# Kernel tuning notes

Hardware: AMD Instinct MI355X
Metric: run time of the kernel (lower is better)

Reference implementation:

```python
import jax, jax.numpy as jnp
import numpy as np

TRIM_RATIO = 0.1
B, N, D_IN, D_H, N_OUT, D_OUT = 64, 1024, 512, 1024, 10, 1


def setup_inputs() -> dict:
    key = jax.random.key(0)
    ks = jax.random.split(key, 10)
    X = jax.random.normal(ks[0], (B, N, D_IN), dtype=jnp.float32)
    # ragged valid lengths in [N//2, N]; guarantees num_valid > 2*k for trim_ratio=0.1
    lengths = jax.random.randint(ks[1], (B,), N // 2, N + 1)
    mask = (jnp.arange(N)[None, :] < lengths[:, None]).astype(jnp.float32)
    s_in, s_h = 1.0 / np.sqrt(D_IN), 1.0 / np.sqrt(D_H)
    W1 = jax.random.uniform(ks[2], (D_IN, D_H), jnp.float32, -s_in, s_in)
    b1 = jax.random.uniform(ks[3], (D_H,), jnp.float32, -s_in, s_in)
    W2 = jax.random.uniform(ks[4], (D_H, D_H), jnp.float32, -s_h, s_h)
    b2 = jax.random.uniform(ks[5], (D_H,), jnp.float32, -s_h, s_h)
    W3 = jax.random.uniform(ks[6], (D_H, D_H), jnp.float32, -s_h, s_h)
    b3 = jax.random.uniform(ks[7], (D_H,), jnp.float32, -s_h, s_h)
    W4 = jax.random.uniform(ks[8], (D_H, N_OUT * D_OUT), jnp.float32, -s_h, s_h)
    b4 = jax.random.uniform(ks[9], (N_OUT * D_OUT,), jnp.float32, -s_h, s_h)
    return {"X": X, "mask": mask, "W1": W1, "b1": b1, "W2": W2, "b2": b2,
            "W3": W3, "b3": b3, "W4": W4, "b4": b4}


def reference(X, mask, W1, b1, W2, b2, W3, b3, W4, b4):
    # encode MLP: [B,N,D_IN] -> [B,N,D_H]
    encoded = jax.nn.relu(jnp.einsum('bni,ih->bnh', X, W1) + b1) @ W2 + b2
    masked = encoded * mask[..., None]
    num_valid = mask.sum(axis=-1).astype(jnp.int32)                 # [B]
    k = (num_valid.astype(jnp.float32) * TRIM_RATIO).astype(jnp.int32)  # floor, as int()
    # push invalid rows to +inf so valid elements occupy the first num_valid slots after sort
    padded = jnp.where(mask[..., None] > 0, masked, jnp.inf)
    sorted_v = jnp.sort(padded, axis=1)                             # per-column sort, [B,N,D_H]
    pos = jnp.arange(N)[None, :]
    keep = (pos >= k[:, None]) & (pos < (num_valid - k)[:, None])   # [B,N]
    summed = jnp.sum(jnp.where(keep[..., None], sorted_v, 0.0), axis=1)  # [B,D_H]
    denom = (num_valid - 2 * k).astype(jnp.float32)[:, None]
    aggregated = summed / denom                                     # trimmed mean
    # decode MLP
    out = jax.nn.relu(aggregated @ W3 + b3) @ W4 + b4               # [B, N_OUT*D_OUT]
    out = out.reshape(-1, N_OUT, D_OUT).squeeze(-1)                 # [B, N_OUT]
    return out
```

## Files before the change

kernel.cpp:

```cpp
#include <hip/hip_runtime.h>


typedef _Float16 half8  __attribute__((ext_vector_type(8)));
typedef _Float16 half4v __attribute__((ext_vector_type(4)));
typedef float    floatx4 __attribute__((ext_vector_type(4)));

#define GLD_LDS(g, l)                                                                     \
  __builtin_amdgcn_global_load_lds((const __attribute__((address_space(1))) void*)(g),    \
                                   (__attribute__((address_space(3))) void*)(l), 16, 0, 0)

__global__ void prep_nv(const float* __restrict__ mask, int* __restrict__ nv_arr,
                        int* __restrict__ k_arr) {
  int b = blockIdx.x, lane = threadIdx.x;
  const float4* mp = (const float4*)(mask + (b << 10));
  float s = 0.f;
#pragma unroll
  for (int i = 0; i < 4; ++i) {
    float4 v = mp[lane + i * 64];
    s += v.x + v.y + v.z + v.w;
  }
#pragma unroll
  for (int off = 32; off > 0; off >>= 1) s += __shfl_xor(s, off, 64);
  if (lane == 0) {
    int nv = (int)(s + 0.5f);
    int kk = (int)((float)nv * 0.1f);
    nv_arr[b] = nv;
    k_arr[b] = kk;
  }
}

__device__ __forceinline__ void transpose_body(const float* __restrict__ W,
                                               _Float16* __restrict__ WT, int R, int C,
                                               int r0, int c0, _Float16 (*tile)[65]) {
  for (int i = threadIdx.x; i < 4096; i += 256) {
    int r = i >> 6, c = i & 63;
    tile[r][c] = (_Float16)W[(size_t)(r0 + r) * C + c0 + c];
  }
  __syncthreads();
  for (int i = threadIdx.x; i < 4096; i += 256) {
    int c = i >> 6, r = i & 63;
    WT[(size_t)(c0 + c) * R + r0 + r] = tile[r][c];
  }
}

__global__ __launch_bounds__(256) void preprocess(
    const float* __restrict__ X, _Float16* __restrict__ X16,
    const float* __restrict__ W1, _Float16* __restrict__ W1T,
    const float* __restrict__ W2, _Float16* __restrict__ W2T,
    const int* __restrict__ nv_arr) {
  __shared__ _Float16 tile[64][65];
  int bid = blockIdx.x;
  if (bid < 16384) {
    int n0 = (bid << 2) & 1023;
    int batch = bid >> 8;
    int nv = nv_arr[batch];
    if (n0 >= ((nv + 127) & ~127)) return;
    int i = (bid * 256 + threadIdx.x) * 8;
    float4 a = *(const float4*)(X + i);
    float4 c = *(const float4*)(X + i + 4);
    half8 h;
    h[0] = (_Float16)a.x; h[1] = (_Float16)a.y; h[2] = (_Float16)a.z; h[3] = (_Float16)a.w;
    h[4] = (_Float16)c.x; h[5] = (_Float16)c.y; h[6] = (_Float16)c.z; h[7] = (_Float16)c.w;
    *(half8*)(X16 + i) = h;
  } else if (bid < 16384 + 128) {
    int id = bid - 16384;
    transpose_body(W1, W1T, 512, 1024, (id & 7) * 64, (id >> 3) * 64, tile);
  } else {
    int id = bid - 16512;
    transpose_body(W2, W2T, 1024, 1024, (id & 15) * 64, (id >> 4) * 64, tile);
  }
}

template <int KDIM, int MODE>
__global__ __launch_bounds__(256, 3) void gemm_kernel_sm(
    const _Float16* __restrict__ Aop, const _Float16* __restrict__ Bop,
    const float* __restrict__ bias, const int* __restrict__ nv_arr,
    _Float16* __restrict__ outp) {
  __shared__ __align__(16) _Float16 ldsA[128 * 64];
  __shared__ __align__(16) _Float16 ldsB[128 * 64];
  int i0, j0;
  int bid = blockIdx.x;
  int fat = (((bid >> 6) << 3) | (bid & 7)) * 128;
  int thin = ((bid >> 3) & 7) * 128;
  if (MODE == 1) {
    i0 = thin; j0 = fat;
    if ((j0 & 1023) >= nv_arr[j0 >> 10]) return;
  } else {
    i0 = fat; j0 = thin;
    if ((i0 & 1023) >= nv_arr[i0 >> 10]) return;
  }
  const int t = threadIdx.x, lane = t & 63;
  const int wv = t >> 6, wi = wv & 1, wj = wv >> 1;
  const int lr = lane & 15, q = lane >> 4;

  floatx4 acc[4][4] = {};

  const int gch = (t & 7) ^ ((t >> 3) & 7);
  const _Float16* gA[4];
  const _Float16* gB[4];
  _Float16* lA[4];
  _Float16* lB[4];
#pragma unroll
  for (int r = 0; r < 4; ++r) {
    int row = r * 32 + (t >> 3);
    gA[r] = Aop + (size_t)(i0 + row) * KDIM + gch * 8;
    gB[r] = Bop + (size_t)(j0 + row) * KDIM + gch * 8;
    lA[r] = ldsA + (r * 256 + (t & ~63)) * 8;
    lB[r] = ldsB + (r * 256 + (t & ~63)) * 8;
  }

  int aoff[4], boff[4];
#pragma unroll
  for (int mi = 0; mi < 4; ++mi) {
    int row = wi * 64 + mi * 16 + lr;
    aoff[mi] = row * 64 + ((q ^ (row & 7)) * 8);
  }
#pragma unroll
  for (int nj = 0; nj < 4; ++nj) {
    int row = wj * 64 + nj * 16 + lr;
    boff[nj] = row * 64 + ((q ^ (row & 7)) * 8);
  }

  for (int kt = 0; kt < KDIM / 64; ++kt) {
#pragma unroll
    for (int r = 0; r < 4; ++r) GLD_LDS(gA[r], lA[r]);
#pragma unroll
    for (int r = 0; r < 4; ++r) GLD_LDS(gB[r], lB[r]);
#pragma unroll
    for (int r = 0; r < 4; ++r) { gA[r] += 64; gB[r] += 64; }
    __syncthreads();
#pragma unroll
    for (int kk = 0; kk < 2; ++kk) {
      half8 af[4], bf[4];
#pragma unroll
      for (int mi = 0; mi < 4; ++mi) af[mi] = *(const half8*)&ldsA[aoff[mi] ^ (kk * 32)];
#pragma unroll
      for (int nj = 0; nj < 4; ++nj) bf[nj] = *(const half8*)&ldsB[boff[nj] ^ (kk * 32)];
#pragma unroll
      for (int mi = 0; mi < 4; ++mi)
#pragma unroll
        for (int nj = 0; nj < 4; ++nj)
          acc[mi][nj] =
              __builtin_amdgcn_mfma_f32_16x16x32_f16(af[mi], bf[nj], acc[mi][nj], 0, 0, 0);
    }
    __syncthreads();
  }

  if (MODE == 1) {
#pragma unroll
    for (int mi = 0; mi < 4; ++mi) {
      int ih = i0 + wi * 64 + mi * 16 + q * 4;
      floatx4 bb = *(const floatx4*)&bias[ih];
#pragma unroll
      for (int nj = 0; nj < 4; ++nj) {
        int j = j0 + wj * 64 + nj * 16 + lr;
        floatx4 v = acc[mi][nj];
        half4v hv;
#pragma unroll
        for (int r = 0; r < 4; ++r) hv[r] = (_Float16)fmaxf(v[r] + bb[r], 0.f);
        *(half4v*)&outp[(size_t)j * 1024 + ih] = hv;
      }
    }
  } else {
#pragma unroll
    for (int nj = 0; nj < 4; ++nj) {
      int j = j0 + wj * 64 + nj * 16 + lr;
      float bj = bias[j];
#pragma unroll
      for (int mi = 0; mi < 4; ++mi) {
        int im = i0 + wi * 64 + mi * 16 + q * 4;
        int bb = im >> 10, n = im & 1023;
        floatx4 v = acc[mi][nj];
        half4v hv;
#pragma unroll
        for (int r = 0; r < 4; ++r) hv[r] = (_Float16)(v[r] + bj);
        *(half4v*)&outp[((size_t)bb << 20) + ((size_t)j << 10) + (size_t)n] = hv;
      }
    }
  }
}

template <int KDIM, int MODE>
__global__ __launch_bounds__(512, 2) void gemm_kernel(
    const _Float16* __restrict__ Aop, const _Float16* __restrict__ Bop,
    const float* __restrict__ bias, const int* __restrict__ nv_arr,
    _Float16* __restrict__ outp) {
  constexpr int NT = KDIM / 64;
  __shared__ __align__(16) _Float16 lds[2][2][256 * 64];

  int bid = blockIdx.x;
  int fat = ((((bid >> 5) << 3) | (bid & 7))) << 8;
  int thin = ((bid >> 3) & 3) << 8;
  int i0, j0;
  if (MODE == 1) {
    i0 = thin; j0 = fat;
    if ((j0 & 1023) >= nv_arr[j0 >> 10]) return;
  } else {
    i0 = fat; j0 = thin;
    if ((i0 & 1023) >= nv_arr[i0 >> 10]) return;
  }
  const int t = threadIdx.x, lane = t & 63;
  const int wv = t >> 6, wm = wv & 1, wn = wv >> 1;
  const int lr = lane & 15, q = lane >> 4;
  const int swz = (q ^ (lr & 7)) * 8;

  const int gch = (t & 7) ^ ((t >> 3) & 7);
  const _Float16* gA = Aop + (size_t)(i0 + (t >> 3)) * KDIM + gch * 8;
  const _Float16* gB = Bop + (size_t)(j0 + (t >> 3)) * KDIM + gch * 8;

#define STG(OP, BUF, KT, R)                                                   \
  GLD_LDS(((OP) ? gB : gA) + (size_t)(R) * 64 * KDIM + (size_t)(KT) * 64,     \
          &lds[BUF][OP][((R) * 512 + (t & ~63)) * 8])

  floatx4 acc[8][4] = {};
  half8 af[4][2];
  half8 bf[2][2][2];

#define LD_A(BUF, IH)                                                         \
  _Pragma("unroll") for (int f = 0; f < 4; ++f)                               \
  _Pragma("unroll") for (int kk = 0; kk < 2; ++kk)                            \
      af[f][kk] = *(const half8*)&lds[BUF][0]                                 \
          [(((wm << 7) + ((IH) << 6) + (f << 4) + lr) << 6) + (swz ^ (kk << 5))];

#define LD_B_HALF(BUF, JH)                                                    \
  _Pragma("unroll") for (int g = 0; g < 2; ++g)                               \
  _Pragma("unroll") for (int kk = 0; kk < 2; ++kk)                            \
      bf[JH][g][kk] = *(const half8*)&lds[BUF][1]                             \
          [(((wn << 6) + ((JH) << 5) + (g << 4) + lr) << 6) + (swz ^ (kk << 5))];

#define MFMA_QUAD(IH, JH)                                                     \
  __builtin_amdgcn_s_setprio(1);                                              \
  _Pragma("unroll") for (int f = 0; f < 4; ++f)                               \
  _Pragma("unroll") for (int g = 0; g < 2; ++g)                               \
  _Pragma("unroll") for (int kk = 0; kk < 2; ++kk)                            \
      acc[((IH) << 2) + f][((JH) << 1) + g] =                                 \
          __builtin_amdgcn_mfma_f32_16x16x32_f16(                             \
              af[f][kk], bf[JH][g][kk], acc[((IH) << 2) + f][((JH) << 1) + g], 0, 0, 0); \
  __builtin_amdgcn_s_setprio(0);

#define TILE(KT, CUR, DO_STG, DO_B1)                                          \
  {                                                                           \
    LD_A(CUR, 0);                                                             \
    LD_B_HALF(CUR, 0);                                                        \
    LD_B_HALF(CUR, 1);                                                        \
    MFMA_QUAD(0, 0);                                                          \
    MFMA_QUAD(0, 1);                                                          \
    LD_A(CUR, 1);                                                             \
    asm volatile("s_waitcnt lgkmcnt(0)" ::: "memory");                        \
    __builtin_amdgcn_sched_barrier(0);                                        \
    __builtin_amdgcn_s_barrier();            \
    __builtin_amdgcn_sched_barrier(0);                                        \
    if (DO_STG) { STG(0, CUR, (KT) + 2, 0); STG(0, CUR, (KT) + 2, 1);         \
                  STG(1, CUR, (KT) + 2, 0); STG(1, CUR, (KT) + 2, 1);         \
                  STG(0, CUR, (KT) + 2, 2); STG(0, CUR, (KT) + 2, 3);         \
                  STG(1, CUR, (KT) + 2, 2); STG(1, CUR, (KT) + 2, 3); }       \
    MFMA_QUAD(1, 0);                                                          \
    MFMA_QUAD(1, 1);                                                          \
    if (DO_B1) {                                                              \
      if (DO_STG) { asm volatile("s_waitcnt vmcnt(8)" ::: "memory"); }        \
      else        { asm volatile("s_waitcnt vmcnt(0)" ::: "memory"); }        \
      __builtin_amdgcn_sched_barrier(0);                                      \
      __builtin_amdgcn_s_barrier();                 \
      __builtin_amdgcn_sched_barrier(0);                                      \
    }                                                                         \
  }

  STG(0, 0, 0, 0); STG(0, 0, 0, 1); STG(0, 0, 0, 2); STG(0, 0, 0, 3);
  STG(1, 0, 0, 0); STG(1, 0, 0, 1); STG(1, 0, 0, 2); STG(1, 0, 0, 3);
  STG(0, 1, 1, 0); STG(0, 1, 1, 1); STG(0, 1, 1, 2); STG(0, 1, 1, 3);
  STG(1, 1, 1, 0); STG(1, 1, 1, 1); STG(1, 1, 1, 2); STG(1, 1, 1, 3);
  asm volatile("s_waitcnt vmcnt(8)" ::: "memory");
  __builtin_amdgcn_s_barrier();
  __builtin_amdgcn_sched_barrier(0);

  for (int kt = 0; kt < NT - 2; kt += 2) {
    TILE(kt, 0, 1, 1);
    TILE(kt + 1, 1, 1, 1);
  }
  TILE(NT - 2, 0, 0, 1);
  TILE(NT - 1, 1, 0, 0);

  if (MODE == 1) {
#pragma unroll
    for (int mi = 0; mi < 8; ++mi) {
      int ih = i0 + (wm << 7) + (mi << 4) + (q << 2);
      floatx4 bb = *(const floatx4*)&bias[ih];
#pragma unroll
      for (int nj = 0; nj < 4; ++nj) {
        int j = j0 + (wn << 6) + (nj << 4) + lr;
        floatx4 v = acc[mi][nj];
        half4v hv;
#pragma unroll
        for (int r = 0; r < 4; ++r) hv[r] = (_Float16)fmaxf(v[r] + bb[r], 0.f);
        *(half4v*)&outp[(size_t)j * 1024 + ih] = hv;
      }
    }
  } else {
#pragma unroll
    for (int nj = 0; nj < 4; ++nj) {
      int j = j0 + (wn << 6) + (nj << 4) + lr;
      float bj = bias[j];
#pragma unroll
      for (int mi = 0; mi < 8; ++mi) {
        int im = i0 + (wm << 7) + (mi << 4) + (q << 2);
        int bb = im >> 10, n = im & 1023;
        floatx4 v = acc[mi][nj];
        half4v hv;
#pragma unroll
        for (int r = 0; r < 4; ++r) hv[r] = (_Float16)(v[r] + bj);
        *(half4v*)&outp[((size_t)bb << 20) + ((size_t)j << 10) + (size_t)n] = hv;
      }
    }
  }
}

#define NB 1024
__global__ __launch_bounds__(256) void trim_kernel(const _Float16* __restrict__ encT,
                                                   const int* __restrict__ nv_arr,
                                                   const int* __restrict__ k_arr,
                                                   float* __restrict__ agg) {
  int t = threadIdx.x, lane = t & 63, w = t >> 6;
  int blk = blockIdx.x;
  int batch = blk >> 8;
  int h = ((blk & 255) << 2) + w;
  int nv = nv_arr[batch], kk = k_arr[batch];
  const _Float16* col = encT + ((size_t)batch << 20) + ((size_t)h << 10);
  const uint4* p = (const uint4*)col;
  uint4 u0 = p[lane];
  uint4 u1 = p[lane + 64];
  unsigned vals[8] = {u0.x, u0.y, u0.z, u0.w, u1.x, u1.y, u1.z, u1.w};

  float vv[16];
  int bn[16];
#pragma unroll
  for (int d = 0; d < 8; ++d) {
    unsigned u = vals[d];
    int pbase = (d < 4) ? (8 * lane + 2 * d) : (512 + 8 * lane + 2 * (d - 4));
#pragma unroll
    for (int sub = 0; sub < 2; ++sub) {
      int idx = 2 * d + sub;
      unsigned short bits = (unsigned short)(sub ? (u >> 16) : (u & 0xffffu));
      _Float16 hvv;
      __builtin_memcpy(&hvv, &bits, 2);
      float v = (float)hvv;
      if (pbase + sub < nv) {
        v = fminf(fmaxf(v, -8.0f), 7.999f);
        int bin = min(NB - 1, (int)((v + 8.0f) * 64.0f));
        vv[idx] = v;
        bn[idx] = bin;
      } else {
        vv[idx] = 0.f;
        bn[idx] = -1;
      }
    }
  }

  int r1 = kk, r2 = nv - kk;
  int b1 = 0, b2 = 0;
#pragma unroll
  for (int s = 512; s > 0; s >>= 1) {
    int cand = b1 + s - 1;
    int c = 0;
#pragma unroll
    for (int i = 0; i < 16; ++i) c += ((unsigned)bn[i] <= (unsigned)cand) ? 1 : 0;
#pragma unroll
    for (int off = 32; off > 0; off >>= 1) c += __shfl_xor(c, off, 64);
    if (c < r1) b1 += s;
  }
#pragma unroll
  for (int s = 512; s > 0; s >>= 1) {
    int cand = b2 + s - 1;
    int c = 0;
#pragma unroll
    for (int i = 0; i < 16; ++i) c += ((unsigned)bn[i] <= (unsigned)cand) ? 1 : 0;
#pragma unroll
    for (int off = 32; off > 0; off >>= 1) c += __shfl_xor(c, off, 64);
    if (c < r2) b2 += s;
  }

  int cex1, cex2;
  {
    int ca = 0, cb = 0;
#pragma unroll
    for (int i = 0; i < 16; ++i) {
      ca += ((unsigned)bn[i] < (unsigned)b1) ? 1 : 0;
      cb += ((unsigned)bn[i] < (unsigned)b2) ? 1 : 0;
    }
    int packed = ca | (cb << 16);
#pragma unroll
    for (int off = 32; off > 0; off >>= 1) packed += __shfl_xor(packed, off, 64);
    cex1 = packed & 0xffff;
    cex2 = packed >> 16;
  }

  float s1 = 0.f, s2 = 0.f, tm = 0.f;
  int c1 = 0, c2 = 0;
#pragma unroll
  for (int i = 0; i < 16; ++i) {
    int b = bn[i];
    float v = vv[i];
    if (b == b1) { s1 += v; c1++; }
    if (b == b2) { s2 += v; c2++; }
    if (b > b1 && b < b2) tm += v;
  }
  int cpk = c1 | (c2 << 16);
#pragma unroll
  for (int off = 32; off > 0; off >>= 1) {
    s1 += __shfl_xor(s1, off, 64);
    s2 += __shfl_xor(s2, off, 64);
    tm += __shfl_xor(tm, off, 64);
    cpk += __shfl_xor(cpk, off, 64);
  }
  c1 = cpk & 0xffff;
  c2 = cpk >> 16;
  float mid;
  if (b1 == b2) {
    mid = (float)(r2 - r1) * (s1 / (float)c1);
  } else {
    mid = (float)(cex1 + c1 - r1) * (s1 / (float)c1) + tm +
          (float)(r2 - cex2) * (s2 / (float)c2);
  }
  if (lane == 0) {
    agg[(batch << 10) + h] = mid / (float)(nv - 2 * kk);
  }
}

__global__ __launch_bounds__(256) void decode1(const float* __restrict__ agg,
                                               const float* __restrict__ W3,
                                               const float* __restrict__ b3,
                                               float* __restrict__ A3) {
  __shared__ float al[1024];
  __shared__ float red[256];
  int b = blockIdx.x, hb = blockIdx.y, t = threadIdx.x;
  for (int i = t; i < 1024; i += 256) al[i] = agg[(b << 10) + i];
  __syncthreads();
  int hl = t & 63, ks = t >> 6;
  int h = hb * 64 + hl;
  const float* wp = W3 + (size_t)(ks * 256) * 1024 + h;
  const float* ap = al + ks * 256;
  float acc = 0.f;
#pragma unroll 8
  for (int k = 0; k < 256; ++k) acc = fmaf(ap[k], wp[(size_t)k * 1024], acc);
  red[t] = acc;
  __syncthreads();
  if (t < 64) {
    float s = red[t] + red[t + 64] + red[t + 128] + red[t + 192] + b3[hb * 64 + t];
    A3[(b << 10) + hb * 64 + t] = fmaxf(s, 0.f);
  }
}

__global__ void decode2(const float* __restrict__ A3, const float* __restrict__ W4,
                        const float* __restrict__ b4, float* __restrict__ outp) {
  __shared__ float red[4][10];
  int b = blockIdx.x, t = threadIdx.x, lane = t & 63, w = t >> 6;
  float part[10];
#pragma unroll
  for (int o = 0; o < 10; ++o) part[o] = 0.f;
#pragma unroll
  for (int jj = 0; jj < 4; ++jj) {
    int h2 = jj * 256 + t;
    float a = A3[(b << 10) + h2];
#pragma unroll
    for (int o = 0; o < 10; ++o) part[o] = fmaf(a, W4[h2 * 10 + o], part[o]);
  }
#pragma unroll
  for (int o = 0; o < 10; ++o)
#pragma unroll
    for (int off = 32; off > 0; off >>= 1) part[o] += __shfl_xor(part[o], off, 64);
  if (lane == 0)
#pragma unroll
    for (int o = 0; o < 10; ++o) red[w][o] = part[o];
  __syncthreads();
  if (t < 10) outp[b * 10 + t] = b4[t] + red[0][t] + red[1][t] + red[2][t] + red[3][t];
}

extern "C" void kernel_launch(void* const* d_in, const int* in_sizes, int n_in,
                              void* d_out, int out_size, void* d_ws, size_t ws_size,
                              hipStream_t stream) {
  const float* X = (const float*)d_in[0];
  const float* mask = (const float*)d_in[1];
  const float* W1 = (const float*)d_in[2];
  const float* b1 = (const float*)d_in[3];
  const float* W2 = (const float*)d_in[4];
  const float* b2 = (const float*)d_in[5];
  const float* W3 = (const float*)d_in[6];
  const float* b3 = (const float*)d_in[7];
  const float* W4 = (const float*)d_in[8];
  const float* b4 = (const float*)d_in[9];
  float* outp = (float*)d_out;
  char* ws = (char*)d_ws;

  _Float16* X16 = (_Float16*)(ws);
  _Float16* H1 = (_Float16*)(ws + 67108864ull);
  _Float16* encT = (_Float16*)(ws + 201326592ull);
  _Float16* W1T = (_Float16*)(ws + 335544320ull);
  _Float16* W2T = (_Float16*)(ws + 336592896ull);
  float* agg = (float*)(ws + 338690048ull);
  float* A3 = (float*)(ws + 338952192ull);
  int* nv_arr = (int*)(ws + 339214336ull);
  int* k_arr = (int*)(ws + 339214592ull);

  prep_nv<<<64, 64, 0, stream>>>(mask, nv_arr, k_arr);
  preprocess<<<16768, 256, 0, stream>>>(X, X16, W1, W1T, W2, W2T, nv_arr);
  gemm_kernel_sm<512, 1><<<4096, 256, 0, stream>>>(W1T, X16, b1, nv_arr, H1);
  gemm_kernel<1024, 2><<<1024, 512, 0, stream>>>(H1, W2T, b2, nv_arr, encT);
  trim_kernel<<<16384, 256, 0, stream>>>(encT, nv_arr, k_arr, agg);
  decode1<<<dim3(64, 16), 256, 0, stream>>>(agg, W3, b3, A3);
  decode2<<<64, 256, 0, stream>>>(A3, W4, b4, outp);
}
```

Measured before the change: 606.8 us.

## Replace binary-search rank selection with LDS histogram and wave prefix scan

The trimmed-mean kernel used to find the boundary bins for ranks k and nv-k with two 10-step binary searches, each needing a 64-lane shuffle reduction. It now builds a per-wave 1024-bin histogram in LDS with atomic adds and XOR-swizzled indexing, then finds both boundary bins with one wave prefix scan and a max-reduction. Each lane now loads 16 contiguous values instead of two strided chunks, which changes the validity check. This adds LDS zeroing, atomic contention, and 16 KB of shared memory per block, which may lower occupancy, in exchange for fewer serial shuffle reductions.

New measurement: 527.7 us. 1.15x faster.

```diff
diff --git a/kernel.cpp b/kernel.cpp
--- a/kernel.cpp
+++ b/kernel.cpp
@@ -319,35 +319,47 @@
                                                    const int* __restrict__ nv_arr,
                                                    const int* __restrict__ k_arr,
                                                    float* __restrict__ agg) {
+  __shared__ unsigned int cnt[4 * NB];
   int t = threadIdx.x, lane = t & 63, w = t >> 6;
   int blk = blockIdx.x;
   int batch = blk >> 8;
   int h = ((blk & 255) << 2) + w;
+  unsigned int* cw = cnt + w * NB;
+  uint4* cp = (uint4*)cw;
+  {
+    uint4 z = {0u, 0u, 0u, 0u};
+#pragma unroll
+    for (int i = 0; i < 4; ++i) cp[lane * 4 + (i ^ ((lane >> 1) & 3))] = z;
+  }
+
   int nv = nv_arr[batch], kk = k_arr[batch];
   const _Float16* col = encT + ((size_t)batch << 20) + ((size_t)h << 10);
-  const uint4* p = (const uint4*)col;
-  uint4 u0 = p[lane];
-  uint4 u1 = p[lane + 64];
+  const uint4* p = (const uint4*)col + lane * 2;
+  uint4 u0 = p[0], u1 = p[1];
   unsigned vals[8] = {u0.x, u0.y, u0.z, u0.w, u1.x, u1.y, u1.z, u1.w};
+  int nvalid = nv - lane * 16;
 
   float vv[16];
   int bn[16];
 #pragma unroll
   for (int d = 0; d < 8; ++d) {
     unsigned u = vals[d];
-    int pbase = (d < 4) ? (8 * lane + 2 * d) : (512 + 8 * lane + 2 * (d - 4));
 #pragma unroll
     for (int sub = 0; sub < 2; ++sub) {
-      int idx = 2 * d + sub;
+      int idx = d * 2 + sub;
       unsigned short bits = (unsigned short)(sub ? (u >> 16) : (u & 0xffffu));
       _Float16 hvv;
       __builtin_memcpy(&hvv, &bits, 2);
       float v = (float)hvv;
-      if (pbase + sub < nv) {
+      if (idx < nvalid) {
         v = fminf(fmaxf(v, -8.0f), 7.999f);
-        int bin = min(NB - 1, (int)((v + 8.0f) * 64.0f));
+        int bin = (int)((v + 8.0f) * 64.0f);
+        bin = min(NB - 1, bin);
         vv[idx] = v;
         bn[idx] = bin;
+        int Lb = bin >> 4, jc = (bin >> 2) & 3;
+        int phys = ((Lb << 2) + (jc ^ ((Lb >> 1) & 3))) * 4 + (bin & 3);
+        atomicAdd(&cw[phys], 1u);
       } else {
         vv[idx] = 0.f;
         bn[idx] = -1;
@@ -355,44 +367,46 @@
     }
   }
 
+  int c[16];
+  {
+    uint4 rb[4];
+#pragma unroll
+    for (int i = 0; i < 4; ++i) rb[i] = cp[lane * 4 + (i ^ ((lane >> 1) & 3))];
+#pragma unroll
+    for (int i = 0; i < 4; ++i) {
+      c[4 * i] = (int)rb[i].x; c[4 * i + 1] = (int)rb[i].y;
+      c[4 * i + 2] = (int)rb[i].z; c[4 * i + 3] = (int)rb[i].w;
+    }
+  }
+  int ct = 0;
+#pragma unroll
+  for (int i = 0; i < 16; ++i) ct += c[i];
+  int ci = ct;
+#pragma unroll
+  for (int off = 1; off < 64; off <<= 1) {
+    int cu = __shfl_up(ci, off, 64);
+    if (lane >= off) ci += cu;
+  }
+  int cex = ci - ct;
   int r1 = kk, r2 = nv - kk;
-  int b1 = 0, b2 = 0;
-#pragma unroll
-  for (int s = 512; s > 0; s >>= 1) {
-    int cand = b1 + s - 1;
-    int c = 0;
-#pragma unroll
-    for (int i = 0; i < 16; ++i) c += ((unsigned)bn[i] <= (unsigned)cand) ? 1 : 0;
-#pragma unroll
-    for (int off = 32; off > 0; off >>= 1) c += __shfl_xor(c, off, 64);
-    if (c < r1) b1 += s;
-  }
-#pragma unroll
-  for (int s = 512; s > 0; s >>= 1) {
-    int cand = b2 + s - 1;
-    int c = 0;
-#pragma unroll
-    for (int i = 0; i < 16; ++i) c += ((unsigned)bn[i] <= (unsigned)cand) ? 1 : 0;
-#pragma unroll
-    for (int off = 32; off > 0; off >>= 1) c += __shfl_xor(c, off, 64);
-    if (c < r2) b2 += s;
-  }
-
-  int cex1, cex2;
+  int p1 = -1, p2 = -1;
   {
-    int ca = 0, cb = 0;
+    int run = cex;
 #pragma unroll
     for (int i = 0; i < 16; ++i) {
-      ca += ((unsigned)bn[i] < (unsigned)b1) ? 1 : 0;
-      cb += ((unsigned)bn[i] < (unsigned)b2) ? 1 : 0;
-    }
-    int packed = ca | (cb << 16);
-#pragma unroll
-    for (int off = 32; off > 0; off >>= 1) packed += __shfl_xor(packed, off, 64);
-    cex1 = packed & 0xffff;
-    cex2 = packed >> 16;
-  }
-
+      int cc = c[i];
+      if (run < r1 && r1 <= run + cc) p1 = ((lane * 16 + i) << 12) | run;
+      if (run < r2 && r2 <= run + cc) p2 = ((lane * 16 + i) << 12) | run;
+      run += cc;
+    }
+  }
+#pragma unroll
+  for (int off = 32; off > 0; off >>= 1) {
+    p1 = max(p1, __shfl_xor(p1, off, 64));
+    p2 = max(p2, __shfl_xor(p2, off, 64));
+  }
+  int b1 = p1 >> 12, cex1 = p1 & 4095;
+  int b2 = p2 >> 12, cex2 = p2 & 4095;
   float s1 = 0.f, s2 = 0.f, tm = 0.f;
   int c1 = 0, c2 = 0;
 #pragma unroll
@@ -403,16 +417,14 @@
     if (b == b2) { s2 += v; c2++; }
     if (b > b1 && b < b2) tm += v;
   }
-  int cpk = c1 | (c2 << 16);
 #pragma unroll
   for (int off = 32; off > 0; off >>= 1) {
     s1 += __shfl_xor(s1, off, 64);
     s2 += __shfl_xor(s2, off, 64);
     tm += __shfl_xor(tm, off, 64);
-    cpk += __shfl_xor(cpk, off, 64);
-  }
-  c1 = cpk & 0xffff;
-  c2 = cpk >> 16;
+    c1 += __shfl_xor(c1, off, 64);
+    c2 += __shfl_xor(c2, off, 64);
+  }
   float mid;
   if (b1 == b2) {
     mid = (float)(r2 - r1) * (s1 / (float)c1);
```
